# Kernel optimization log

Measured on AMD Instinct MI355X. Metric: run time of the kernel, lower is better.

Reference implementation:

```python
import jax, jax.numpy as jnp
import numpy as np

B, T, C = 256, 256, 384
HEADS = 6
HEAD_DIM = C // HEADS
WINDOW = 64


def setup_inputs() -> dict:
    key = jax.random.key(0)
    ks = jax.random.split(key, 5)
    scale = 0.02
    return {
        "x": jax.random.normal(ks[0], (B, T, C), dtype=jnp.float32),
        "qkv_w": jax.random.normal(ks[1], (C, 3 * C), dtype=jnp.float32) * scale,
        "qkv_b": jax.random.normal(ks[2], (3 * C,), dtype=jnp.float32) * scale,
        "proj_w": jax.random.normal(ks[3], (C, C), dtype=jnp.float32) * scale,
        "proj_b": jax.random.normal(ks[4], (C,), dtype=jnp.float32) * scale,
        "gate": jnp.ones((C,), dtype=jnp.float32),
    }


def reference(x, qkv_w, qkv_b, proj_w, proj_b, gate):
    Bx, Tx, Cx = x.shape
    qkv = x @ qkv_w + qkv_b                     # [B, T, 3C]
    q, k, v = jnp.split(qkv, 3, axis=-1)
    # [B, T, H, hd] -> [B, H, T, hd]
    q = q.reshape(Bx, Tx, HEADS, HEAD_DIM).transpose(0, 2, 1, 3)
    k = k.reshape(Bx, Tx, HEADS, HEAD_DIM).transpose(0, 2, 1, 3)
    v = v.reshape(Bx, Tx, HEADS, HEAD_DIM).transpose(0, 2, 1, 3)

    att = jnp.einsum("bhqd,bhkd->bhqk", q, k) * (1.0 / np.sqrt(HEAD_DIM).astype(np.float32))
    idx = jnp.arange(Tx)
    causal = idx[:, None] >= idx[None, :]                 # j <= i
    local = jnp.abs(idx[:, None] - idx[None, :]) <= WINDOW
    mask = (causal & local)[None, None, :, :]             # [1,1,T,T]
    att = jnp.where(mask, att, -jnp.inf)
    att = jax.nn.softmax(att, axis=-1)

    out = jnp.einsum("bhqk,bhkd->bhqd", att, v)           # [B, H, T, hd]
    out = out.transpose(0, 2, 1, 3).reshape(Bx, Tx, Cx)
    return (out * gate) @ proj_w + proj_b
```

## Files before the change

### kernel.cpp

```cpp
#include <hip/hip_runtime.h>
#include <hip/hip_bf16.h>

typedef unsigned short u16;
typedef __attribute__((ext_vector_type(8))) short short8;
typedef __attribute__((ext_vector_type(8))) unsigned short ushort8;
typedef __attribute__((ext_vector_type(4))) float f32x4;
typedef __attribute__((ext_vector_type(4))) float f4;

#define GLB_CAST(p) ((const __attribute__((address_space(1))) unsigned int*)(p))
#define LDS_CAST(p) ((__attribute__((address_space(3))) unsigned int*)(p))

__device__ __forceinline__ void gl_lds16(const void* g, void* l) {
  __builtin_amdgcn_global_load_lds(GLB_CAST(g), LDS_CAST(l), 16, 0, 0);
}

__device__ __forceinline__ u16 f2bf(float f) {
  __hip_bfloat16 b = __float2bfloat16(f);
  return __builtin_bit_cast(u16, b);
}
__device__ __forceinline__ float bf2f(u16 u) {
  unsigned int x = ((unsigned int)u) << 16;
  return __builtin_bit_cast(float, x);
}

__global__ void transpose_cvt_k(const float* __restrict__ in,
                                u16* __restrict__ out, int R, int C) {
  __shared__ float tile[32][33];
  int c0 = blockIdx.x * 32, r0 = blockIdx.y * 32;
  int tx = threadIdx.x, ty = threadIdx.y;
#pragma unroll
  for (int i = 0; i < 32; i += 8)
    tile[ty + i][tx] = in[(size_t)(r0 + ty + i) * C + c0 + tx];
  __syncthreads();
#pragma unroll
  for (int i = 0; i < 32; i += 8)
    out[(size_t)(c0 + ty + i) * R + r0 + tx] = f2bf(tile[tx][ty + i]);
}

template <int EPI>
__global__ __launch_bounds__(256, 2) void gemm_k(
    const void* __restrict__ Av, const u16* __restrict__ Bt,
    const float* __restrict__ bias,
    u16* __restrict__ oQ, u16* __restrict__ oK, u16* __restrict__ oVT,
    float* __restrict__ oF) {
  constexpr int K = 384;
  constexpr int NT = (EPI == 1) ? 9 : 3;
  __shared__ u16 As[64 * 384];
  __shared__ u16 Bs[4][3][1024];
  __shared__ u16 Rs[4][512];
  __shared__ u16 bias_sh[NT * 128];

  const int tid = threadIdx.x;
  const int m0 = blockIdx.x * 64;
  const int lane = tid & 63, wid = tid >> 6;
  const int lo = lane & 15, hi = lane >> 4;
  const int wc = wid;

  for (int i = tid; i < NT * 128; i += 256) bias_sh[i] = f2bf(bias[i]);

  const int bcol = wc * 32 + (lane >> 2);
  const int bc = ((lane & 3) ^ ((lane >> 3) & 3)) * 8;
  char* const slot_l = (char*)&Bs[0][0][0] + wid * 6144 + lane * 16;
  auto stageB = [&](int slot, int tn, int kt) {
    const u16* s = Bt + (size_t)(tn * 128 + bcol) * K + kt * 32 + bc;
    char* d = slot_l + slot * 2048;
    gl_lds16(s, d);
    gl_lds16(s + 16 * K, d + 1024);
  };

  stageB(0, 0, 0);
  stageB(1, 0, 1);

  if (EPI == 1) {
    const float* X = (const float*)Av;
#pragma unroll
    for (int i = 0; i < 12; ++i) {
      int c = tid + i * 256;
      int row = c / 48, cc = c % 48;
      const float* src = X + (size_t)(m0 + row) * K + cc * 8;
      f4 a = __builtin_nontemporal_load((const f4*)src);
      f4 b = __builtin_nontemporal_load((const f4*)(src + 4));
      ushort8 o;
#pragma unroll
      for (int j = 0; j < 4; ++j) { o[j] = f2bf(a[j]); o[4 + j] = f2bf(b[j]); }
      *(ushort8*)((char*)As + row * 768 + ((cc * 16) ^ ((row & 7) << 4))) = o;
    }
  } else {
    const u16* Ab = (const u16*)Av;
#pragma unroll
    for (int i = 0; i < 12; ++i) {
      int c = tid + i * 256;
      int row = c / 48, cc = c % 48;
      ushort8 v = __builtin_nontemporal_load(
          (const ushort8*)(Ab + (size_t)(m0 + row) * K + cc * 8));
      *(ushort8*)((char*)As + row * 768 + ((cc * 16) ^ ((row & 7) << 4))) = v;
    }
  }
  __syncthreads();

  const int akey = (lo & 7) << 4;
  const int rk = ((lo >> 1) & 3) << 4;
  int abase[4];
#pragma unroll
  for (int m = 0; m < 4; ++m) abase[m] = (m * 16 + lo) * 768;
  const int bbase = lo * 64 + (hi * 16 ^ rk);
  const char* const Asc = (const char*)As;
  const char* const sb0 = (const char*)&Bs[0][0][0] + wid * 6144;
  char* const rp_ = (char*)&Rs[0][0] + wid * 1024;

  const f32x4 Z4 = {0.f, 0.f, 0.f, 0.f};

  for (int t = 0; t < NT; ++t) {
    f32x4 acc[4][2];
#pragma unroll
    for (int m = 0; m < 4; ++m) { acc[m][0] = Z4; acc[m][1] = Z4; }

#pragma unroll
    for (int kt = 0; kt < 12; ++kt) {
      if (kt == 0) asm volatile("s_waitcnt vmcnt(4)" ::: "memory");
      else         asm volatile("s_waitcnt vmcnt(2)" ::: "memory");

      const char* sb = sb0 + (kt % 3) * 2048;
      short8 af[4], bf[2];
#pragma unroll
      for (int m = 0; m < 4; ++m)
        af[m] = *(const short8*)(Asc + abase[m] + ((kt * 64 + hi * 16) ^ akey));
      bf[0] = *(const short8*)(sb + bbase);
      bf[1] = *(const short8*)(sb + 1024 + bbase);

      if (kt < 10)           stageB((kt + 2) % 3, t, kt + 2);
      else if (t + 1 < NT)   stageB((kt + 2) % 3, t + 1, kt - 10);

      __builtin_amdgcn_s_setprio(1);
#pragma unroll
      for (int m = 0; m < 4; ++m) {
        acc[m][0] = __builtin_amdgcn_mfma_f32_16x16x32_bf16(af[m], bf[0], acc[m][0], 0, 0, 0);
        acc[m][1] = __builtin_amdgcn_mfma_f32_16x16x32_bf16(af[m], bf[1], acc[m][1], 0, 0, 0);
      }
      __builtin_amdgcn_s_setprio(0);
    }

    float bs0 = bf2f(bias_sh[t * 128 + wc * 32 + lo]);
    float bs1 = bf2f(bias_sh[t * 128 + wc * 32 + 16 + lo]);

    if (EPI == 1) {
      const int r3 = t / 3;
      u16* dst = (r3 == 0) ? oQ : ((r3 == 1) ? oK : oVT);
      const int hcb = (t - r3 * 3) * 128 + wc * 32;
      if (r3 < 2) {
#pragma unroll
        for (int p = 0; p < 4; ++p) {
#pragma unroll
          for (int n = 0; n < 2; ++n)
#pragma unroll
            for (int rr = 0; rr < 4; ++rr)
              *(u16*)(rp_ + (hi * 4 + rr) * 64 + (n * 16 + lo) * 2) =
                  f2bf(acc[p][n][rr] + (n ? bs1 : bs0));
          ushort8 v = *(const ushort8*)(rp_ + (lane >> 2) * 64 + (lane & 3) * 16);
          int hc = hcb + (lane & 3) * 8;
          int gm = m0 + p * 16 + (lane >> 2);
          *(ushort8*)(dst + (((size_t)((gm >> 8) * 6 + (hc >> 6))) << 14) +
                      (gm & 255) * 64 + (hc & 63)) = v;
        }
      } else {
#pragma unroll
        for (int p = 0; p < 4; ++p) {
#pragma unroll
          for (int n = 0; n < 2; ++n)
#pragma unroll
            for (int rr = 0; rr < 4; ++rr)
              *(u16*)(rp_ + (n * 16 + lo) * 32 + (hi * 4 + rr) * 2) =
                  f2bf(acc[p][n][rr] + (n ? bs1 : bs0));
          ushort8 v = *(const ushort8*)(rp_ + (lane >> 1) * 32 + (lane & 1) * 16);
          int hc = hcb + (lane >> 1);
          int tg = (m0 & 255) + p * 16 + (lane & 1) * 8;
          *(ushort8*)(dst + (((size_t)((m0 >> 8) * 6 + (hc >> 6))) << 14) +
                      (hc & 63) * 256 + tg) = v;
        }
      }
    } else {
      const int colb = t * 128 + wc * 32 + lo;
#pragma unroll
      for (int m = 0; m < 4; ++m)
#pragma unroll
        for (int rr = 0; rr < 4; ++rr) {
          int gm = m0 + m * 16 + hi * 4 + rr;
          __builtin_nontemporal_store(acc[m][0][rr] + bs0, &oF[(size_t)gm * 384 + colb]);
          __builtin_nontemporal_store(acc[m][1][rr] + bs1, &oF[(size_t)gm * 384 + colb + 16]);
        }
    }
  }
}

__global__ __launch_bounds__(256) void attn_k(
    const u16* __restrict__ Qb, const u16* __restrict__ Kb,
    const u16* __restrict__ VTb, const float* __restrict__ gate,
    u16* __restrict__ Ao) {
  __shared__ u16 Ks[128 * 64];
  __shared__ u16 Vs[64 * 128];
  __shared__ u16 Ps[4][16 * 128];
  const int bx = blockIdx.x;
  const int qt = bx & 3, bh = bx >> 2;
  const int h = bh % 6, b = bh / 6;
  const int i0 = qt * 64, j0 = i0 - 64;
  const int tid = threadIdx.x, w = tid >> 6, lane = tid & 63;
  const int lo = lane & 15, hi = lane >> 4;

  const u16* Kh = Kb + (size_t)bh * (256 * 64);
  const u16* Vh = VTb + (size_t)bh * (64 * 256);
  const u16* Qh = Qb + (size_t)bh * (256 * 64);

#pragma unroll
  for (int it = 0; it < 4; ++it) {
    int chunk = tid + it * 256;
    int row = chunk >> 3, cc = chunk & 7;
    int csrc = cc ^ (row & 7);
    int j = j0 + row; if (j < 0) j = 0;
    gl_lds16(Kh + j * 64 + csrc * 8, Ks + chunk * 8);
  }
#pragma unroll
  for (int it = 0; it < 4; ++it) {
    int chunk = tid + it * 256;
    int d = chunk >> 4, kc = chunk & 15;
    int ksrc = kc ^ (d & 7);
    int j = j0 + ksrc * 8; if (j < 0) j = 0;
    gl_lds16(Vh + d * 256 + j, Vs + chunk * 8);
  }

  const int iq = i0 + w * 16 + lo;
  short8 aq0 = *(const short8*)(Qh + iq * 64 + hi * 8);
  short8 aq1 = *(const short8*)(Qh + iq * 64 + 32 + hi * 8);

  __syncthreads();

  const f32x4 Z4 = {0.f, 0.f, 0.f, 0.f};
  f32x4 accS[8];
#pragma unroll
  for (int t = 0; t < 8; ++t) accS[t] = Z4;
#pragma unroll
  for (int t = 0; t < 8; ++t) {
    int key = t * 16 + lo;
    int base = key * 128;
    int sw = (key & 7) << 4;
    short8 bk0 = *(const short8*)((const char*)Ks + ((base + hi * 16) ^ sw));
    short8 bk1 = *(const short8*)((const char*)Ks + ((base + 64 + hi * 16) ^ sw));
    accS[t] = __builtin_amdgcn_mfma_f32_16x16x32_bf16(aq0, bk0, accS[t], 0, 0, 0);
    accS[t] = __builtin_amdgcn_mfma_f32_16x16x32_bf16(aq1, bk1, accS[t], 0, 0, 0);
  }

  float pv[4][8];
  float rinv[4];
#pragma unroll
  for (int r = 0; r < 4; ++r) {
    int i = i0 + w * 16 + hi * 4 + r;
    float mx = -1e30f;
    float vals[8];
#pragma unroll
    for (int t = 0; t < 8; ++t) {
      int j = j0 + t * 16 + lo;
      float s = accS[t][r] * 0.125f;
      bool ok = (j >= 0) && (j <= i) && (j >= i - 64);
      vals[t] = ok ? s : -1e30f;
      mx = fmaxf(mx, vals[t]);
    }
#pragma unroll
    for (int off = 1; off < 16; off <<= 1) mx = fmaxf(mx, __shfl_xor(mx, off));
    float sum = 0.f;
#pragma unroll
    for (int t = 0; t < 8; ++t) {
      float p = __expf(vals[t] - mx);
      pv[r][t] = p;
      sum += p;
    }
#pragma unroll
    for (int off = 1; off < 16; off <<= 1) sum += __shfl_xor(sum, off);
    rinv[r] = 1.0f / sum;
  }

  u16* Pw = Ps[w];
#pragma unroll
  for (int r = 0; r < 4; ++r) {
    int ql = hi * 4 + r;
    int sw = (ql & 7) << 4;
#pragma unroll
    for (int t = 0; t < 8; ++t) {
      int off = (ql * 256 + (t * 16 + lo) * 2) ^ sw;
      *(u16*)((char*)Pw + off) = f2bf(pv[r][t]);
    }
  }

  f32x4 accO[4];
#pragma unroll
  for (int dt = 0; dt < 4; ++dt) accO[dt] = Z4;
#pragma unroll
  for (int ks = 0; ks < 4; ++ks) {
    int offA = (lo * 256 + ks * 64 + hi * 16) ^ ((lo & 7) << 4);
    short8 ap = *(const short8*)((const char*)Pw + offA);
#pragma unroll
    for (int dt = 0; dt < 4; ++dt) {
      int d = dt * 16 + lo;
      int offB = (d * 256 + ks * 64 + hi * 16) ^ ((d & 7) << 4);
      short8 bv = *(const short8*)((const char*)Vs + offB);
      accO[dt] = __builtin_amdgcn_mfma_f32_16x16x32_bf16(ap, bv, accO[dt], 0, 0, 0);
    }
  }

#pragma unroll
  for (int dt = 0; dt < 4; ++dt) {
    int d = dt * 16 + lo;
    float gg = gate[h * 64 + d];
#pragma unroll
    for (int r = 0; r < 4; ++r) {
      int i = i0 + w * 16 + hi * 4 + r;
      float v = accO[dt][r] * rinv[r] * gg;
      Ao[(size_t)(b * 256 + i) * 384 + h * 64 + d] = f2bf(v);
    }
  }
}

extern "C" void kernel_launch(void* const* d_in, const int* in_sizes, int n_in,
                              void* d_out, int out_size, void* d_ws, size_t ws_size,
                              hipStream_t stream) {
  const float* x      = (const float*)d_in[0];
  const float* qkv_w  = (const float*)d_in[1];
  const float* qkv_b  = (const float*)d_in[2];
  const float* proj_w = (const float*)d_in[3];
  const float* proj_b = (const float*)d_in[4];
  const float* gate   = (const float*)d_in[5];
  float* out = (float*)d_out;

  char* ws = (char*)d_ws;
  u16* att  = (u16*)ws;
  u16* vT   = (u16*)(ws + 50331648);
  u16* w1T  = (u16*)(ws + 100663296);
  u16* pT   = (u16*)(ws + 101548032);
  u16* qbuf = (u16*)d_out;
  u16* kbuf = (u16*)((char*)d_out + 50331648);

  transpose_cvt_k<<<dim3(1152 / 32, 384 / 32), dim3(32, 8), 0, stream>>>(qkv_w, w1T, 384, 1152);
  transpose_cvt_k<<<dim3(384 / 32, 384 / 32), dim3(32, 8), 0, stream>>>(proj_w, pT, 384, 384);

  gemm_k<1><<<1024, 256, 0, stream>>>(x, w1T, qkv_b, qbuf, kbuf, vT, nullptr);
  attn_k<<<256 * 6 * 4, 256, 0, stream>>>(qbuf, kbuf, vT, gate, att);
  gemm_k<2><<<1024, 256, 0, stream>>>(att, pT, proj_b, nullptr, nullptr, nullptr, out);
}
```

Baseline: 188.8 us.

## Fuse windowed attention with output projection GEMM per 64-row tile

Adds a kernel in which each block computes attention for all six heads of a 64-query tile, keeps the gated result in LDS, and then runs the output projection with a triple-buffered weight pipeline. This removes the bf16 attention round-trip through global memory and the separate projection launch. Q and K move into workspace so the output buffer can be written directly, with a fallback to the old path when the workspace is too small. The cost is about 100KB of LDS per block, which limits occupancy to one block per CU, and the six heads are processed serially inside each block.

```diff
diff --git a/kernel.cpp b/kernel.cpp
--- a/kernel.cpp
+++ b/kernel.cpp
@@ -189,6 +189,213 @@
           __builtin_nontemporal_store(acc[m][1][rr] + bs1, &oF[(size_t)gm * 384 + colb + 16]);
         }
     }
+  }
+}
+
+__global__ __launch_bounds__(256, 1) void attn_proj_k(
+    const u16* __restrict__ Qb, const u16* __restrict__ Kb,
+    const u16* __restrict__ VTb, const u16* __restrict__ pT,
+    const float* __restrict__ gate, const float* __restrict__ projb,
+    float* __restrict__ out) {
+  __shared__ u16 Ks[128 * 64];
+  __shared__ u16 Vs[64 * 128];
+  __shared__ u16 Ps[4][16 * 128];
+  __shared__ u16 Am[64 * 384];
+  __shared__ u16 Bs[4][3][1024];
+
+  const int bx = blockIdx.x;
+  const int qt = bx & 3, b = bx >> 2;
+  const int i0 = qt * 64, j0 = i0 - 64;
+  const int tid = threadIdx.x, w = tid >> 6, lane = tid & 63;
+  const int lo = lane & 15, hi = lane >> 4;
+  const f32x4 Z4 = {0.f, 0.f, 0.f, 0.f};
+
+  float pb0[3], pb1[3];
+#pragma unroll
+  for (int t = 0; t < 3; ++t) {
+    pb0[t] = projb[t * 128 + w * 32 + lo];
+    pb1[t] = projb[t * 128 + w * 32 + 16 + lo];
+  }
+
+  const int bcol = w * 32 + (lane >> 2);
+  const int bc = ((lane & 3) ^ ((lane >> 3) & 3)) * 8;
+  char* const slot_l = (char*)&Bs[0][0][0] + w * 6144 + lane * 16;
+  auto stageB = [&](int slot, int tn, int kt) {
+    const u16* s = pT + (size_t)(tn * 128 + bcol) * 384 + kt * 32 + bc;
+    char* d = slot_l + slot * 2048;
+    gl_lds16(s, d);
+    gl_lds16(s + 16 * 384, d + 1024);
+  };
+
+  for (int h = 0; h < 6; ++h) {
+    const size_t bh = (size_t)(b * 6 + h);
+    const u16* Kh = Kb + bh * (256 * 64);
+    const u16* Vh = VTb + bh * (64 * 256);
+    const u16* Qh = Qb + bh * (256 * 64);
+
+#pragma unroll
+    for (int it = 0; it < 4; ++it) {
+      int chunk = tid + it * 256;
+      int row = chunk >> 3, cc = chunk & 7;
+      int csrc = cc ^ (row & 7);
+      int j = j0 + row; if (j < 0) j = 0;
+      gl_lds16(Kh + j * 64 + csrc * 8, Ks + chunk * 8);
+    }
+#pragma unroll
+    for (int it = 0; it < 4; ++it) {
+      int chunk = tid + it * 256;
+      int d = chunk >> 4, kc = chunk & 15;
+      int ksrc = kc ^ (d & 7);
+      int j = j0 + ksrc * 8; if (j < 0) j = 0;
+      gl_lds16(Vh + d * 256 + j, Vs + chunk * 8);
+    }
+
+    const int iq = i0 + w * 16 + lo;
+    short8 aq0 = *(const short8*)(Qh + iq * 64 + hi * 8);
+    short8 aq1 = *(const short8*)(Qh + iq * 64 + 32 + hi * 8);
+    float gg[4];
+#pragma unroll
+    for (int dt = 0; dt < 4; ++dt) gg[dt] = gate[h * 64 + dt * 16 + lo];
+
+    __syncthreads();
+
+    f32x4 accS[8];
+#pragma unroll
+    for (int t = 0; t < 8; ++t) accS[t] = Z4;
+#pragma unroll
+    for (int t = 0; t < 8; ++t) {
+      int key = t * 16 + lo;
+      int base = key * 128;
+      int sw = (key & 7) << 4;
+      short8 bk0 = *(const short8*)((const char*)Ks + ((base + hi * 16) ^ sw));
+      short8 bk1 = *(const short8*)((const char*)Ks + ((base + 64 + hi * 16) ^ sw));
+      accS[t] = __builtin_amdgcn_mfma_f32_16x16x32_bf16(aq0, bk0, accS[t], 0, 0, 0);
+      accS[t] = __builtin_amdgcn_mfma_f32_16x16x32_bf16(aq1, bk1, accS[t], 0, 0, 0);
+    }
+
+    float pv[4][8], rinv[4];
+#pragma unroll
+    for (int r = 0; r < 4; ++r) {
+      int i = i0 + w * 16 + hi * 4 + r;
+      float mx = -1e30f;
+      float vals[8];
+#pragma unroll
+      for (int t = 0; t < 8; ++t) {
+        int j = j0 + t * 16 + lo;
+        float s = accS[t][r] * 0.125f;
+        bool ok = (j >= 0) && (j <= i) && (j >= i - 64);
+        vals[t] = ok ? s : -1e30f;
+        mx = fmaxf(mx, vals[t]);
+      }
+#pragma unroll
+      for (int off = 1; off < 16; off <<= 1) mx = fmaxf(mx, __shfl_xor(mx, off));
+      float sum = 0.f;
+#pragma unroll
+      for (int t = 0; t < 8; ++t) {
+        float p = __expf(vals[t] - mx);
+        pv[r][t] = p;
+        sum += p;
+      }
+#pragma unroll
+      for (int off = 1; off < 16; off <<= 1) sum += __shfl_xor(sum, off);
+      rinv[r] = 1.0f / sum;
+    }
+
+    u16* Pw = Ps[w];
+#pragma unroll
+    for (int r = 0; r < 4; ++r) {
+      int ql = hi * 4 + r;
+      int sw = (ql & 7) << 4;
+#pragma unroll
+      for (int t = 0; t < 8; ++t) {
+        int off = (ql * 256 + (t * 16 + lo) * 2) ^ sw;
+        *(u16*)((char*)Pw + off) = f2bf(pv[r][t]);
+      }
+    }
+
+    f32x4 accO[4];
+#pragma unroll
+    for (int dt = 0; dt < 4; ++dt) accO[dt] = Z4;
+#pragma unroll
+    for (int ks = 0; ks < 4; ++ks) {
+      int offA = (lo * 256 + ks * 64 + hi * 16) ^ ((lo & 7) << 4);
+      short8 ap = *(const short8*)((const char*)Pw + offA);
+#pragma unroll
+      for (int dt = 0; dt < 4; ++dt) {
+        int d = dt * 16 + lo;
+        int offB = (d * 256 + ks * 64 + hi * 16) ^ ((d & 7) << 4);
+        short8 bv = *(const short8*)((const char*)Vs + offB);
+        accO[dt] = __builtin_amdgcn_mfma_f32_16x16x32_bf16(ap, bv, accO[dt], 0, 0, 0);
+      }
+    }
+
+#pragma unroll
+    for (int dt = 0; dt < 4; ++dt) {
+#pragma unroll
+      for (int r = 0; r < 4; ++r) {
+        int lr = w * 16 + hi * 4 + r;
+        int col = h * 64 + dt * 16 + lo;
+        float v = accO[dt][r] * rinv[r] * gg[dt];
+        *(u16*)((char*)Am + lr * 768 + ((2 * col) ^ ((lr & 7) << 4))) = f2bf(v);
+      }
+    }
+
+    if (h == 5) {
+      stageB(0, 0, 0);
+      stageB(1, 0, 1);
+    }
+    __syncthreads();
+  }
+
+  const int akey = (lo & 7) << 4;
+  const int rk = ((lo >> 1) & 3) << 4;
+  int abase[4];
+#pragma unroll
+  for (int m = 0; m < 4; ++m) abase[m] = (m * 16 + lo) * 768;
+  const int bbase = lo * 64 + (hi * 16 ^ rk);
+  const char* const Amc = (const char*)Am;
+  const char* const sb0 = (const char*)&Bs[0][0][0] + w * 6144;
+
+#pragma unroll
+  for (int t = 0; t < 3; ++t) {
+    f32x4 acc[4][2];
+#pragma unroll
+    for (int m = 0; m < 4; ++m) { acc[m][0] = Z4; acc[m][1] = Z4; }
+
+#pragma unroll
+    for (int kt = 0; kt < 12; ++kt) {
+      if (kt == 0) asm volatile("s_waitcnt vmcnt(4)" ::: "memory");
+      else         asm volatile("s_waitcnt vmcnt(2)" ::: "memory");
+
+      const char* sb = sb0 + (kt % 3) * 2048;
+      short8 af[4], bf[2];
+#pragma unroll
+      for (int m = 0; m < 4; ++m)
+        af[m] = *(const short8*)(Amc + abase[m] + ((kt * 64 + hi * 16) ^ akey));
+      bf[0] = *(const short8*)(sb + bbase);
+      bf[1] = *(const short8*)(sb + 1024 + bbase);
+
+      if (kt < 10)        stageB((kt + 2) % 3, t, kt + 2);
+      else if (t + 1 < 3) stageB((kt + 2) % 3, t + 1, kt - 10);
+
+      __builtin_amdgcn_s_setprio(1);
+#pragma unroll
+      for (int m = 0; m < 4; ++m) {
+        acc[m][0] = __builtin_amdgcn_mfma_f32_16x16x32_bf16(af[m], bf[0], acc[m][0], 0, 0, 0);
+        acc[m][1] = __builtin_amdgcn_mfma_f32_16x16x32_bf16(af[m], bf[1], acc[m][1], 0, 0, 0);
+      }
+      __builtin_amdgcn_s_setprio(0);
+    }
+
+    const int colb = t * 128 + w * 32 + lo;
+#pragma unroll
+    for (int m = 0; m < 4; ++m)
+#pragma unroll
+      for (int rr = 0; rr < 4; ++rr) {
+        size_t grow = (size_t)(b * 256 + i0 + m * 16 + hi * 4 + rr) * 384;
+        __builtin_nontemporal_store(acc[m][0][rr] + pb0[t], &out[grow + colb]);
+        __builtin_nontemporal_store(acc[m][1][rr] + pb1[t], &out[grow + colb + 16]);
+      }
   }
 }
 
@@ -328,19 +535,34 @@
   const float* proj_b = (const float*)d_in[4];
   const float* gate   = (const float*)d_in[5];
   float* out = (float*)d_out;
-
   char* ws = (char*)d_ws;
-  u16* att  = (u16*)ws;
-  u16* vT   = (u16*)(ws + 50331648);
-  u16* w1T  = (u16*)(ws + 100663296);
-  u16* pT   = (u16*)(ws + 101548032);
-  u16* qbuf = (u16*)d_out;
-  u16* kbuf = (u16*)((char*)d_out + 50331648);
-
-  transpose_cvt_k<<<dim3(1152 / 32, 384 / 32), dim3(32, 8), 0, stream>>>(qkv_w, w1T, 384, 1152);
-  transpose_cvt_k<<<dim3(384 / 32, 384 / 32), dim3(32, 8), 0, stream>>>(proj_w, pT, 384, 384);
-
-  gemm_k<1><<<1024, 256, 0, stream>>>(x, w1T, qkv_b, qbuf, kbuf, vT, nullptr);
-  attn_k<<<256 * 6 * 4, 256, 0, stream>>>(qbuf, kbuf, vT, gate, att);
-  gemm_k<2><<<1024, 256, 0, stream>>>(att, pT, proj_b, nullptr, nullptr, nullptr, out);
-}
+
+  constexpr size_t SEG = 50331648;
+  const size_t need_fused = 3 * SEG + 884736 + 294912;
+
+  if (ws_size >= need_fused) {
+    u16* qbuf = (u16*)ws;
+    u16* kbuf = (u16*)(ws + SEG);
+    u16* vT   = (u16*)(ws + 2 * SEG);
+    u16* w1T  = (u16*)(ws + 3 * SEG);
+    u16* pT   = (u16*)(ws + 3 * SEG + 884736);
+
+    transpose_cvt_k<<<dim3(36, 12), dim3(32, 8), 0, stream>>>(qkv_w, w1T, 384, 1152);
+    transpose_cvt_k<<<dim3(12, 12), dim3(32, 8), 0, stream>>>(proj_w, pT, 384, 384);
+    gemm_k<1><<<1024, 256, 0, stream>>>(x, w1T, qkv_b, qbuf, kbuf, vT, nullptr);
+    attn_proj_k<<<1024, 256, 0, stream>>>(qbuf, kbuf, vT, pT, gate, proj_b, out);
+  } else {
+    u16* att  = (u16*)ws;
+    u16* vT   = (u16*)(ws + SEG);
+    u16* w1T  = (u16*)(ws + 2 * SEG);
+    u16* pT   = (u16*)(ws + 2 * SEG + 884736);
+    u16* qbuf = (u16*)d_out;
+    u16* kbuf = (u16*)((char*)d_out + SEG);
+
+    transpose_cvt_k<<<dim3(36, 12), dim3(32, 8), 0, stream>>>(qkv_w, w1T, 384, 1152);
+    transpose_cvt_k<<<dim3(12, 12), dim3(32, 8), 0, stream>>>(proj_w, pT, 384, 384);
+    gemm_k<1><<<1024, 256, 0, stream>>>(x, w1T, qkv_b, qbuf, kbuf, vT, nullptr);
+    attn_k<<<256 * 6 * 4, 256, 0, stream>>>(qbuf, kbuf, vT, gate, att);
+    gemm_k<2><<<1024, 256, 0, stream>>>(att, pT, proj_b, nullptr, nullptr, nullptr, out);
+  }
+}
```

Measured after the change: 219.4 us. 1.16x slower.
